# Kernel tuning notes

Measured on AMD Instinct MI355X. Metric: run time of the kernel, lower is better.

The kernel has to match this reference:

```python
import jax, jax.numpy as jnp
import numpy as np

N = 50000      # nodes
F_IN = 1024    # raw feature dim
D = 64         # student_dim = hidden_dim * compression_ratio
P = 3          # number of meta-paths
E = 1600000    # edges per meta-path adjacency (avg degree 32)


def setup_inputs() -> dict:
    key = jax.random.key(0)
    ks = jax.random.split(key, 10)
    feats = jax.random.normal(ks[0], (N, F_IN), jnp.float32)
    rows = jax.random.randint(ks[1], (P, E), 0, N, dtype=jnp.int32)
    cols = jax.random.randint(ks[2], (P, E), 0, N, dtype=jnp.int32)
    # normalized-adjacency-like positive edge weights
    vals = jax.random.uniform(ks[3], (P, E), jnp.float32) / 32.0
    # fc_list[0]: Linear(F_IN -> D), xavier_normal gain=1.414
    W0 = jax.random.normal(ks[4], (D, F_IN), jnp.float32) * 0.05
    b0 = jnp.zeros((D,), jnp.float32)
    # P GCN linear layers (D -> D, no bias) + GCN bias params
    Wg = jax.random.normal(ks[5], (P, D, D), jnp.float32) * 0.17
    bg = jnp.zeros((P, D), jnp.float32)
    # PReLU alpha (torch default init 0.25, one scalar per GCN)
    alpha = jnp.full((P,), 0.25, jnp.float32)
    # Attention: Linear(D -> D) and att vector [1, D]
    Wa = jax.random.normal(ks[6], (D, D), jnp.float32) * 0.17
    ba = jnp.zeros((D,), jnp.float32)
    att = jax.random.normal(ks[7], (1, D), jnp.float32) * 0.17
    return dict(feats=feats, rows=rows, cols=cols, vals=vals, W0=W0, b0=b0,
                Wg=Wg, bg=bg, alpha=alpha, Wa=Wa, ba=ba, att=att)


def reference(feats, rows, cols, vals, W0, b0, Wg, bg, alpha, Wa, ba, att):
    # h = elu(fc_list[0](feats))  (feat_drop = 0 -> identity)
    h = jax.nn.elu(feats @ W0.T + b0)                       # [N, D]
    embeds = []
    for i in range(P):
        s = h @ Wg[i].T                                     # [N, D]
        # sparse adj (COO) @ s : out[r] += v * s[c]
        msg = vals[i][:, None] * s[cols[i]]                 # [E, D]
        out = jax.ops.segment_sum(msg, rows[i], num_segments=N)
        out = out + bg[i]
        embeds.append(jnp.where(out > 0, out, alpha[i] * out))  # PReLU
    emb = jnp.stack(embeds)                                 # [P, N, D]
    # Attention over views: beta_i = att . mean_n tanh(fc(emb_i))
    sp = jnp.tanh(jnp.einsum('pnd,ed->pne', emb, Wa) + ba).mean(axis=1)  # [P, D]
    beta = jax.nn.softmax(sp @ att[0])                      # [P]
    z_mp = jnp.einsum('p,pnd->nd', beta, emb)               # [N, D]
    return z_mp
```

## Files before the change

### kernel.cpp

```cpp
#include <hip/hip_runtime.h>
#include <hip/hip_bf16.h>

#define N_NODES 50000
#define F_IN    1024
#define DD      64
#define PP      3
#define EE      1600000
#define NPC     98
#define CCAP    17664

typedef __attribute__((ext_vector_type(8))) short short8v;
typedef __attribute__((ext_vector_type(4))) float floatx4;
typedef __attribute__((ext_vector_type(2))) float floatx2;

__device__ inline float bfl(uint u) { return __uint_as_float(u << 16); }
__device__ inline float bfh(uint u) { return __uint_as_float(u & 0xffff0000u); }
__device__ inline floatx2 up2(uint u) {
    floatx2 r; r.x = bfl(u); r.y = bfh(u); return r;
}
__device__ inline uint cvtpk2(float a, float b) {
    __hip_bfloat162 h = __float22bfloat162_rn(make_float2(a, b));
    return *(uint*)&h;
}
__device__ inline ushort f2bf(float x) {
    __hip_bfloat16 h = __float2bfloat16(x);
    return *(ushort*)&h;
}

__global__ __launch_bounds__(256) void split_weights(const float* __restrict__ W0,
                                                     const float* __restrict__ Wg,
                                                     const float* __restrict__ Wa,
                                                     ushort* __restrict__ W0h,
                                                     ushort* __restrict__ Wgh,
                                                     ushort* __restrict__ Wah)
{
    int i = blockIdx.x * 256 + threadIdx.x;
    if (i < 64 * 1024) W0h[i] = f2bf(W0[i]);
    int j = i - 64 * 1024;
    if (j >= 0 && j < PP * 64 * 64) Wgh[j] = f2bf(Wg[j]);
    int k = i - 64 * 1024 - PP * 64 * 64;
    if (k >= 0 && k < 64 * 64) Wah[k] = f2bf(Wa[k]);
}

__global__ __launch_bounds__(256) void gemm1_fused(const float* __restrict__ feats,
                                                   const ushort* __restrict__ W0h,
                                                   const float* __restrict__ b0,
                                                   const ushort* __restrict__ Wgh,
                                                   ushort* __restrict__ s_all)
{
    __shared__ ushort Ah[64 * 64];
    __shared__ ushort Bh[64 * 64];
    const int t = threadIdx.x;
    const int w = t >> 6, lane = t & 63;
    const int row0 = blockIdx.x * 64;
    const int l15 = lane & 15, l4 = lane >> 4;

    floatx4 acc[4] = {};
    float4 pa[4];
    uint4  pb[2];

    #pragma unroll
    for (int rep = 0; rep < 4; ++rep) {
        int idx = rep * 256 + t;
        int r = idx >> 4, c4 = idx & 15;
        int gr = row0 + r; if (gr >= N_NODES) gr = N_NODES - 1;
        pa[rep] = *(const float4*)&feats[(size_t)gr * F_IN + c4 * 4];
    }
    #pragma unroll
    for (int rep = 0; rep < 2; ++rep) {
        int idx = rep * 256 + t;
        int c = idx >> 3, u8 = idx & 7;
        pb[rep] = *(const uint4*)&W0h[(size_t)c * F_IN + u8 * 8];
    }

    for (int kc = 0; kc < 16; ++kc) {
        #pragma unroll
        for (int rep = 0; rep < 4; ++rep) {
            int idx = rep * 256 + t;
            int r = idx >> 4, c4 = idx & 15;
            int unit = (c4 >> 1) ^ (r & 7);
            int base = r * 64 + unit * 8 + (c4 & 1) * 4;
            *(uint2*)&Ah[base] = make_uint2(cvtpk2(pa[rep].x, pa[rep].y),
                                            cvtpk2(pa[rep].z, pa[rep].w));
        }
        #pragma unroll
        for (int rep = 0; rep < 2; ++rep) {
            int idx = rep * 256 + t;
            int c = idx >> 3, u8 = idx & 7;
            int unit = u8 ^ (c & 7);
            *(uint4*)&Bh[c * 64 + unit * 8] = pb[rep];
        }
        __syncthreads();

        if (kc < 15) {
            #pragma unroll
            for (int rep = 0; rep < 4; ++rep) {
                int idx = rep * 256 + t;
                int r = idx >> 4, c4 = idx & 15;
                int gr = row0 + r; if (gr >= N_NODES) gr = N_NODES - 1;
                pa[rep] = *(const float4*)&feats[(size_t)gr * F_IN + (kc + 1) * 64 + c4 * 4];
            }
            #pragma unroll
            for (int rep = 0; rep < 2; ++rep) {
                int idx = rep * 256 + t;
                int c = idx >> 3, u8 = idx & 7;
                pb[rep] = *(const uint4*)&W0h[(size_t)c * F_IN + (kc + 1) * 64 + u8 * 8];
            }
        }

        #pragma unroll
        for (int ks = 0; ks < 2; ++ks) {
            int arow = w * 16 + l15;
            int au = (ks * 4 + l4) ^ (arow & 7);
            short8v ah = *(short8v*)&Ah[arow * 64 + au * 8];
            #pragma unroll
            for (int cf = 0; cf < 4; ++cf) {
                int bcol = cf * 16 + l15;
                int bu = (ks * 4 + l4) ^ (bcol & 7);
                short8v bh = *(short8v*)&Bh[bcol * 64 + bu * 8];
                acc[cf] = __builtin_amdgcn_mfma_f32_16x16x32_bf16(ah, bh, acc[cf], 0, 0, 0);
            }
        }
        __syncthreads();
    }

    #pragma unroll
    for (int cf = 0; cf < 4; ++cf) {
        int col = cf * 16 + l15;
        #pragma unroll
        for (int r = 0; r < 4; ++r) {
            int row = w * 16 + l4 * 4 + r;
            float x = acc[cf][r] + b0[col];
            x = x > 0.f ? x : (__expf(x) - 1.f);
            int u = (col >> 3) ^ (row & 7);
            Ah[row * 64 + u * 8 + (col & 7)] = f2bf(x);
        }
    }
    __syncthreads();

    for (int p = 0; p < PP; ++p) {
        #pragma unroll
        for (int rep = 0; rep < 2; ++rep) {
            int idx = rep * 256 + t;
            int r = idx >> 3, u8 = idx & 7;
            int unit = u8 ^ (r & 7);
            *(uint4*)&Bh[r * 64 + unit * 8] = *(const uint4*)&Wgh[(size_t)p * 4096 + idx * 8];
        }
        __syncthreads();

        floatx4 sacc[4] = {};
        #pragma unroll
        for (int ks = 0; ks < 2; ++ks) {
            int arow = w * 16 + l15;
            int au = (ks * 4 + l4) ^ (arow & 7);
            short8v ah = *(short8v*)&Ah[arow * 64 + au * 8];
            #pragma unroll
            for (int cf = 0; cf < 4; ++cf) {
                int bcol = cf * 16 + l15;
                int bu = (ks * 4 + l4) ^ (bcol & 7);
                short8v bh = *(short8v*)&Bh[bcol * 64 + bu * 8];
                sacc[cf] = __builtin_amdgcn_mfma_f32_16x16x32_bf16(ah, bh, sacc[cf], 0, 0, 0);
            }
        }
        ushort* sp = s_all + (size_t)p * N_NODES * 64;
        #pragma unroll
        for (int cf = 0; cf < 4; ++cf) {
            int col = cf * 16 + l15;
            #pragma unroll
            for (int r = 0; r < 4; ++r) {
                int gr = row0 + w * 16 + l4 * 4 + r;
                if (gr < N_NODES)
                    sp[(size_t)gr * 64 + col] = f2bf(sacc[cf][r]);
            }
        }
        __syncthreads();
    }
}

__global__ __launch_bounds__(256) void part1(const int*   __restrict__ rows,
                                             const int*   __restrict__ cols,
                                             const float* __restrict__ vals,
                                             int*   __restrict__ pcur3,
                                             uint2* __restrict__ coarsebuf)
{
    __shared__ uint2 stage[2560];
    __shared__ uint2 sorted[2560];
    __shared__ int cnt[128];
    __shared__ int sc[128];
    __shared__ int curb[128];
    __shared__ int gbase[128];
    const int t = threadIdx.x;
    const int path = blockIdx.y;
    const size_t ebase = (size_t)path * EE + (size_t)blockIdx.x * 2560;
    int* pcur = pcur3 + path * NPC;
    uint2* cb = coarsebuf + (size_t)path * NPC * CCAP;

    if (t < 128) { cnt[t] = 0; curb[t] = 0; }
    __syncthreads();

    #pragma unroll
    for (int it = 0; it < 10; ++it) {
        int e = it * 256 + t;
        int r = rows[ebase + e];
        int c = cols[ebase + e];
        float v = vals[ebase + e];
        int bin = r >> 9, rl = r & 511;
        stage[e] = make_uint2((uint)c | ((uint)rl << 16) | ((uint)bin << 25),
                              __float_as_uint(v));
        atomicAdd(&cnt[bin], 1);
    }
    __syncthreads();

    if (t < 128) sc[t] = cnt[t];
    __syncthreads();
    #pragma unroll
    for (int o = 1; o < 128; o <<= 1) {
        int v = (t < 128 && t >= o) ? sc[t - o] : 0;
        __syncthreads();
        if (t < 128 && t >= o) sc[t] += v;
        __syncthreads();
    }

    if (t < NPC) gbase[t] = atomicAdd(&pcur[t], cnt[t]);
    __syncthreads();

    #pragma unroll
    for (int it = 0; it < 10; ++it) {
        uint2 e = stage[it * 256 + t];
        int bin = e.x >> 25;
        int loc = (sc[bin] - cnt[bin]) + atomicAdd(&curb[bin], 1);
        sorted[loc] = e;
    }
    __syncthreads();

    #pragma unroll
    for (int it = 0; it < 10; ++it) {
        int i = it * 256 + t;
        uint2 e = sorted[i];
        int bin = e.x >> 25;
        int g = gbase[bin] + (i - (sc[bin] - cnt[bin]));
        if (g < CCAP) cb[(size_t)bin * CCAP + g] = e;
    }
}

__global__ __launch_bounds__(512) void sort2(const uint2* __restrict__ coarsebuf,
                                             const int*   __restrict__ pcur3,
                                             uint* __restrict__ sortpk,
                                             int* __restrict__ rowbeg3,
                                             int* __restrict__ rowend3)
{
    __shared__ int hist[512];
    __shared__ int cur[512];
    const int t = threadIdx.x;
    const int c = blockIdx.x, path = blockIdx.y;
    const int n = min(pcur3[path * NPC + c], CCAP);
    const size_t slabbase = ((size_t)path * NPC + c) * CCAP;
    const uint2* src = coarsebuf + slabbase;

    hist[t] = 0;
    __syncthreads();

    for (int i = t; i < n; i += 512)
        atomicAdd(&hist[(src[i].x >> 16) & 511], 1);
    __syncthreads();

    int c0 = hist[t];
    __syncthreads();
    #pragma unroll
    for (int o = 1; o < 512; o <<= 1) {
        int v = (t >= o) ? hist[t - o] : 0;
        __syncthreads();
        hist[t] += v;
        __syncthreads();
    }
    int excl = hist[t] - c0;
    cur[t] = excl;
    int gr = c * 512 + t;
    if (gr < N_NODES) {
        rowbeg3[path * N_NODES + gr] = (int)(slabbase + excl);
        rowend3[path * N_NODES + gr] = (int)(slabbase + excl + c0);
    }
    __syncthreads();

    for (int i = t; i < n; i += 512) {
        uint2 e = src[i];
        int rl = (e.x >> 16) & 511;
        int pos = atomicAdd(&cur[rl], 1);
        sortpk[slabbase + pos] = (e.x & 0xffffu) |
                                 ((uint)f2bf(__uint_as_float(e.y)) << 16);
    }
}

__global__ __launch_bounds__(256) void spmm_gather(const uint*   __restrict__ sortpk,
                                                   const int*    __restrict__ rowbeg3,
                                                   const int*    __restrict__ rowend3,
                                                   const ushort* __restrict__ s_all,
                                                   const float*  __restrict__ bg,
                                                   const float*  __restrict__ alpha,
                                                   ushort* __restrict__ emb)
{
    const int path = blockIdx.x / 12500;
    const int wid = (blockIdx.x % 12500) * 4 + (threadIdx.x >> 6);
    const int lane = threadIdx.x & 63;
    const int dq = lane & 7;
    const int slot = lane >> 3;
    const int e0 = rowbeg3[path * N_NODES + wid];
    const int e1 = rowend3[path * N_NODES + wid];
    const ushort* s_p = s_all + (size_t)path * N_NODES * 64;

    floatx2 acc[4] = {};
    if (e0 < e1) {
        const int last = e1 - 1;
        for (int e = e0; e < e1; e += 32) {
            int ea = e + slot, eb = ea + 8, ec = ea + 16, ed = ea + 24;
            uint pka = sortpk[min(ea, last)];
            uint pkb = sortpk[min(eb, last)];
            uint pkc = sortpk[min(ec, last)];
            uint pkd = sortpk[min(ed, last)];
            const uint4 ga = *(const uint4*)&s_p[(size_t)(pka & 0xffffu) * 64 + dq * 8];
            const uint4 gb = *(const uint4*)&s_p[(size_t)(pkb & 0xffffu) * 64 + dq * 8];
            const uint4 gc = *(const uint4*)&s_p[(size_t)(pkc & 0xffffu) * 64 + dq * 8];
            const uint4 gd = *(const uint4*)&s_p[(size_t)(pkd & 0xffffu) * 64 + dq * 8];
            float va = (ea <= last) ? bfh(pka) : 0.f;
            float vb = (eb <= last) ? bfh(pkb) : 0.f;
            float vc = (ec <= last) ? bfh(pkc) : 0.f;
            float vd = (ed <= last) ? bfh(pkd) : 0.f;
            floatx2 va2 = {va, va}, vb2 = {vb, vb}, vc2 = {vc, vc}, vd2 = {vd, vd};
            acc[0] += va2 * up2(ga.x); acc[1] += va2 * up2(ga.y);
            acc[2] += va2 * up2(ga.z); acc[3] += va2 * up2(ga.w);
            acc[0] += vb2 * up2(gb.x); acc[1] += vb2 * up2(gb.y);
            acc[2] += vb2 * up2(gb.z); acc[3] += vb2 * up2(gb.w);
            acc[0] += vc2 * up2(gc.x); acc[1] += vc2 * up2(gc.y);
            acc[2] += vc2 * up2(gc.z); acc[3] += vc2 * up2(gc.w);
            acc[0] += vd2 * up2(gd.x); acc[1] += vd2 * up2(gd.y);
            acc[2] += vd2 * up2(gd.z); acc[3] += vd2 * up2(gd.w);
        }
    }
    #pragma unroll
    for (int j = 0; j < 4; ++j) {
        acc[j].x += __shfl_xor(acc[j].x, 8);
        acc[j].y += __shfl_xor(acc[j].y, 8);
        acc[j].x += __shfl_xor(acc[j].x, 16);
        acc[j].y += __shfl_xor(acc[j].y, 16);
        acc[j].x += __shfl_xor(acc[j].x, 32);
        acc[j].y += __shfl_xor(acc[j].y, 32);
    }

    if (slot == 0) {
        const float al = alpha[path];
        const float* bgp = bg + path * 64;
        float x[8];
        #pragma unroll
        for (int j = 0; j < 4; ++j) {
            float v0 = acc[j].x + bgp[dq * 8 + 2 * j];
            float v1 = acc[j].y + bgp[dq * 8 + 2 * j + 1];
            x[2 * j]     = v0 > 0.f ? v0 : al * v0;
            x[2 * j + 1] = v1 > 0.f ? v1 : al * v1;
        }
        uint4 wv;
        wv.x = cvtpk2(x[0], x[1]);
        wv.y = cvtpk2(x[2], x[3]);
        wv.z = cvtpk2(x[4], x[5]);
        wv.w = cvtpk2(x[6], x[7]);
        *(uint4*)&emb[((size_t)path * N_NODES + wid) * 64 + dq * 8] = wv;
    }
}

__global__ __launch_bounds__(256) void postproc(const ushort* __restrict__ emb,
                                                const ushort* __restrict__ Wah,
                                                const float* __restrict__ ba,
                                                float* __restrict__ sp)
{
    __shared__ ushort Ah[64 * 64];
    __shared__ ushort Bh[64 * 64];
    __shared__ float red[16][64];
    const int t = threadIdx.x;
    const int w = t >> 6, lane = t & 63;
    const int l15 = lane & 15, l4 = lane >> 4;
    const int nb = (N_NODES + 63) >> 6;
    const int p  = blockIdx.x / nb;
    const int tb = blockIdx.x % nb;
    const int row0 = tb * 64;
    const ushort* embp = emb + (size_t)p * N_NODES * 64;

    #pragma unroll
    for (int rep = 0; rep < 2; ++rep) {
        int idx = rep * 256 + t;
        int r = idx >> 3, u8 = idx & 7;
        int gr = row0 + r; if (gr >= N_NODES) gr = N_NODES - 1;
        int unit = u8 ^ (r & 7);
        *(uint4*)&Ah[r * 64 + unit * 8] = *(const uint4*)&embp[(size_t)gr * 64 + u8 * 8];
        *(uint4*)&Bh[r * 64 + unit * 8] = *(const uint4*)&Wah[idx * 8];
    }
    __syncthreads();

    floatx4 acc[4] = {};
    #pragma unroll
    for (int ks = 0; ks < 2; ++ks) {
        int arow = w * 16 + l15;
        int au = (ks * 4 + l4) ^ (arow & 7);
        short8v ah = *(short8v*)&Ah[arow * 64 + au * 8];
        #pragma unroll
        for (int cf = 0; cf < 4; ++cf) {
            int bcol = cf * 16 + l15;
            int bu = (ks * 4 + l4) ^ (bcol & 7);
            short8v bh = *(short8v*)&Bh[bcol * 64 + bu * 8];
            acc[cf] = __builtin_amdgcn_mfma_f32_16x16x32_bf16(ah, bh, acc[cf], 0, 0, 0);
        }
    }

    #pragma unroll
    for (int cf = 0; cf < 4; ++cf) {
        int col = cf * 16 + l15;
        float s = 0.f;
        #pragma unroll
        for (int r = 0; r < 4; ++r) {
            int gr = row0 + w * 16 + l4 * 4 + r;
            if (gr < N_NODES) s += tanhf(acc[cf][r] + ba[col]);
        }
        red[w * 4 + l4][col] = s;
    }
    __syncthreads();
    if (t < 64) {
        float ssum = 0.f;
        #pragma unroll
        for (int g = 0; g < 16; ++g) ssum += red[g][t];
        unsafeAtomicAdd(&sp[p * 64 + t], ssum);
    }
}

__global__ void beta_kernel(const float* __restrict__ sp,
                            const float* __restrict__ att,
                            float* __restrict__ beta)
{
    int lane = threadIdx.x;
    float w[PP];
    #pragma unroll
    for (int p = 0; p < PP; ++p) {
        float x = sp[p * 64 + lane] * (1.0f / (float)N_NODES) * att[lane];
        #pragma unroll
        for (int off = 32; off; off >>= 1) x += __shfl_down(x, off);
        w[p] = __shfl(x, 0);
    }
    if (lane == 0) {
        float mx = fmaxf(w[0], fmaxf(w[1], w[2]));
        float e0 = __expf(w[0] - mx);
        float e1 = __expf(w[1] - mx);
        float e2 = __expf(w[2] - mx);
        float s = e0 + e1 + e2;
        beta[0] = e0 / s; beta[1] = e1 / s; beta[2] = e2 / s;
    }
}

__global__ __launch_bounds__(256) void combine(const ushort* __restrict__ emb,
                                               const float* __restrict__ beta,
                                               float* __restrict__ out)
{
    const float b0 = beta[0], b1 = beta[1], b2 = beta[2];
    const size_t tot = (size_t)N_NODES * 64;
    size_t i = ((size_t)blockIdx.x * 256 + threadIdx.x) * 8;
    if (i < tot) {
        uint4 e0 = *(const uint4*)&emb[i];
        uint4 e1 = *(const uint4*)&emb[tot + i];
        uint4 e2 = *(const uint4*)&emb[2 * tot + i];
        float o[8];
        o[0] = b0*bfl(e0.x) + b1*bfl(e1.x) + b2*bfl(e2.x);
        o[1] = b0*bfh(e0.x) + b1*bfh(e1.x) + b2*bfh(e2.x);
        o[2] = b0*bfl(e0.y) + b1*bfl(e1.y) + b2*bfl(e2.y);
        o[3] = b0*bfh(e0.y) + b1*bfh(e1.y) + b2*bfh(e2.y);
        o[4] = b0*bfl(e0.z) + b1*bfl(e1.z) + b2*bfl(e2.z);
        o[5] = b0*bfh(e0.z) + b1*bfh(e1.z) + b2*bfh(e2.z);
        o[6] = b0*bfl(e0.w) + b1*bfl(e1.w) + b2*bfl(e2.w);
        o[7] = b0*bfh(e0.w) + b1*bfh(e1.w) + b2*bfh(e2.w);
        *(float4*)&out[i]     = make_float4(o[0], o[1], o[2], o[3]);
        *(float4*)&out[i + 4] = make_float4(o[4], o[5], o[6], o[7]);
    }
}

extern "C" void kernel_launch(void* const* d_in, const int* in_sizes, int n_in,
                              void* d_out, int out_size, void* d_ws, size_t ws_size,
                              hipStream_t stream)
{
    const float* feats = (const float*)d_in[0];
    const int*   rows  = (const int*)  d_in[1];
    const int*   cols  = (const int*)  d_in[2];
    const float* vals  = (const float*)d_in[3];
    const float* W0    = (const float*)d_in[4];
    const float* b0    = (const float*)d_in[5];
    const float* Wg    = (const float*)d_in[6];
    const float* bg    = (const float*)d_in[7];
    const float* alpha = (const float*)d_in[8];
    const float* Wa    = (const float*)d_in[9];
    const float* ba    = (const float*)d_in[10];
    const float* att   = (const float*)d_in[11];
    float* out = (float*)d_out;

    const size_t ND = (size_t)N_NODES * 64;
    char* base = (char*)d_ws;
    ushort* emb    = (ushort*)base;              base += 3 * ND * 2;
    ushort* s_all  = (ushort*)base;              base += 3 * ND * 2;
    ushort* W0h    = (ushort*)base;              base += 64 * 1024 * 2;
    ushort* Wgh    = (ushort*)base;              base += PP * 64 * 64 * 2;
    ushort* Wah    = (ushort*)base;              base += 64 * 64 * 2;
    int*    pcur3  = (int*)base;                 base += PP * NPC * 4;
    float*  sp     = (float*)base;               base += 192 * 4;
    float*  beta   = (float*)base;               base += 64 * 4;
    int*    rowbeg3 = (int*)base;                base += PP * N_NODES * 4;
    int*    rowend3 = (int*)base;                base += PP * N_NODES * 4;
    base = (char*)(((size_t)base + 255) & ~(size_t)255);
    uint2*  coarsebuf = (uint2*)base;            base += (size_t)PP * NPC * CCAP * 8;
    uint*   sortpk    = (uint*)base;             base += (size_t)PP * NPC * CCAP * 4;

    hipMemsetAsync(pcur3, 0, (PP * NPC + 192) * sizeof(int), stream);

    split_weights<<<(64 * 1024 + PP * 64 * 64 + 64 * 64 + 255) / 256, 256, 0, stream>>>(
        W0, Wg, Wa, W0h, Wgh, Wah);

    gemm1_fused<<<782, 256, 0, stream>>>(feats, W0h, b0, Wgh, s_all);

    part1<<<dim3(EE / 2560, 3), 256, 0, stream>>>(rows, cols, vals, pcur3, coarsebuf);
    sort2<<<dim3(NPC, 3), 512, 0, stream>>>(coarsebuf, pcur3, sortpk, rowbeg3, rowend3);
    spmm_gather<<<3 * 12500, 256, 0, stream>>>(
        sortpk, rowbeg3, rowend3, s_all, bg, alpha, emb);

    postproc<<<3 * 782, 256, 0, stream>>>(emb, Wah, ba, sp);
    beta_kernel<<<1, 64, 0, stream>>>(sp, att, beta);
    combine<<<(int)((ND / 8 + 255) / 256), 256, 0, stream>>>(emb, beta, out);
}
```

Before: 316.8 us.

## Split first GEMM along K into two partial-sum blocks, combine in second kernel

The fused feats@W0 GEMM is split into two halves of the K=1024 dimension, launched as a 782x2 grid that writes fp32 partial tiles to a workspace buffer. A new combine kernel sums the partials, applies bias and ELU, and runs the three per-path 64x64 GEMMs. It also stages outputs through shared memory so they can be written as coalesced 16-byte stores. The aim is to double the block count for better CU occupancy on the bandwidth-bound feats read, at the cost of an extra kernel launch and about 25 MB of partial-sum traffic.

```diff
diff --git a/kernel.cpp b/kernel.cpp
--- a/kernel.cpp
+++ b/kernel.cpp
@@ -42,17 +42,16 @@
     if (k >= 0 && k < 64 * 64) Wah[k] = f2bf(Wa[k]);
 }
 
-__global__ __launch_bounds__(256) void gemm1_fused(const float* __restrict__ feats,
-                                                   const ushort* __restrict__ W0h,
-                                                   const float* __restrict__ b0,
-                                                   const ushort* __restrict__ Wgh,
-                                                   ushort* __restrict__ s_all)
+__global__ __launch_bounds__(256) void gemm1_partial(const float* __restrict__ feats,
+                                                     const ushort* __restrict__ W0h,
+                                                     float* __restrict__ hpart)
 {
     __shared__ ushort Ah[64 * 64];
     __shared__ ushort Bh[64 * 64];
     const int t = threadIdx.x;
     const int w = t >> 6, lane = t & 63;
     const int row0 = blockIdx.x * 64;
+    const int kh = blockIdx.y;
     const int l15 = lane & 15, l4 = lane >> 4;
 
     floatx4 acc[4] = {};
@@ -64,16 +63,16 @@
         int idx = rep * 256 + t;
         int r = idx >> 4, c4 = idx & 15;
         int gr = row0 + r; if (gr >= N_NODES) gr = N_NODES - 1;
-        pa[rep] = *(const float4*)&feats[(size_t)gr * F_IN + c4 * 4];
+        pa[rep] = *(const float4*)&feats[(size_t)gr * F_IN + (kh * 8) * 64 + c4 * 4];
     }
     #pragma unroll
     for (int rep = 0; rep < 2; ++rep) {
         int idx = rep * 256 + t;
         int c = idx >> 3, u8 = idx & 7;
-        pb[rep] = *(const uint4*)&W0h[(size_t)c * F_IN + u8 * 8];
-    }
-
-    for (int kc = 0; kc < 16; ++kc) {
+        pb[rep] = *(const uint4*)&W0h[(size_t)c * F_IN + (kh * 8) * 64 + u8 * 8];
+    }
+
+    for (int kc = 0; kc < 8; ++kc) {
         #pragma unroll
         for (int rep = 0; rep < 4; ++rep) {
             int idx = rep * 256 + t;
@@ -92,19 +91,20 @@
         }
         __syncthreads();
 
-        if (kc < 15) {
+        if (kc < 7) {
+            int g = kh * 8 + kc + 1;
             #pragma unroll
             for (int rep = 0; rep < 4; ++rep) {
                 int idx = rep * 256 + t;
                 int r = idx >> 4, c4 = idx & 15;
                 int gr = row0 + r; if (gr >= N_NODES) gr = N_NODES - 1;
-                pa[rep] = *(const float4*)&feats[(size_t)gr * F_IN + (kc + 1) * 64 + c4 * 4];
+                pa[rep] = *(const float4*)&feats[(size_t)gr * F_IN + g * 64 + c4 * 4];
             }
             #pragma unroll
             for (int rep = 0; rep < 2; ++rep) {
                 int idx = rep * 256 + t;
                 int c = idx >> 3, u8 = idx & 7;
-                pb[rep] = *(const uint4*)&W0h[(size_t)c * F_IN + (kc + 1) * 64 + u8 * 8];
+                pb[rep] = *(const uint4*)&W0h[(size_t)c * F_IN + g * 64 + u8 * 8];
             }
         }
 
@@ -124,13 +124,41 @@
         __syncthreads();
     }
 
+    float* hp = hpart + ((size_t)(kh * 782 + blockIdx.x)) * 4096;
+    #pragma unroll
+    for (int cf = 0; cf < 4; ++cf)
+        *(float4*)&hp[(cf * 256 + t) * 4] = make_float4(acc[cf][0], acc[cf][1],
+                                                        acc[cf][2], acc[cf][3]);
+}
+
+__global__ __launch_bounds__(256) void gemm2_combine(const float* __restrict__ hpart,
+                                                     const float* __restrict__ b0,
+                                                     const ushort* __restrict__ Wgh,
+                                                     ushort* __restrict__ s_all)
+{
+    __shared__ ushort Ah[64 * 64];
+    __shared__ ushort Bh[64 * 64];
+    __shared__ ushort Sout[64 * 64];
+    const int t = threadIdx.x;
+    const int w = t >> 6, lane = t & 63;
+    const int row0 = blockIdx.x * 64;
+    const int l15 = lane & 15, l4 = lane >> 4;
+
+    const float* hp0 = hpart + (size_t)blockIdx.x * 4096;
+    const float* hp1 = hpart + (size_t)(782 + blockIdx.x) * 4096;
+
     #pragma unroll
     for (int cf = 0; cf < 4; ++cf) {
+        float4 a = *(const float4*)&hp0[(cf * 256 + t) * 4];
+        float4 b = *(const float4*)&hp1[(cf * 256 + t) * 4];
         int col = cf * 16 + l15;
+        float bias = b0[col];
+        float xs[4] = {a.x + b.x + bias, a.y + b.y + bias,
+                       a.z + b.z + bias, a.w + b.w + bias};
         #pragma unroll
         for (int r = 0; r < 4; ++r) {
             int row = w * 16 + l4 * 4 + r;
-            float x = acc[cf][r] + b0[col];
+            float x = xs[r];
             x = x > 0.f ? x : (__expf(x) - 1.f);
             int u = (col >> 3) ^ (row & 7);
             Ah[row * 64 + u * 8 + (col & 7)] = f2bf(x);
@@ -162,15 +190,22 @@
                 sacc[cf] = __builtin_amdgcn_mfma_f32_16x16x32_bf16(ah, bh, sacc[cf], 0, 0, 0);
             }
         }
-        ushort* sp = s_all + (size_t)p * N_NODES * 64;
         #pragma unroll
         for (int cf = 0; cf < 4; ++cf) {
             int col = cf * 16 + l15;
             #pragma unroll
-            for (int r = 0; r < 4; ++r) {
-                int gr = row0 + w * 16 + l4 * 4 + r;
-                if (gr < N_NODES)
-                    sp[(size_t)gr * 64 + col] = f2bf(sacc[cf][r]);
+            for (int r = 0; r < 4; ++r)
+                Sout[(w * 16 + l4 * 4 + r) * 64 + col] = f2bf(sacc[cf][r]);
+        }
+        __syncthreads();
+        {
+            int lr = t >> 2;
+            int gr = row0 + lr;
+            if (gr < N_NODES) {
+                ushort* sp = s_all + (size_t)p * N_NODES * 64;
+                int co = (t & 3) * 16;
+                *(uint4*)&sp[(size_t)gr * 64 + co]     = *(uint4*)&Sout[lr * 64 + co];
+                *(uint4*)&sp[(size_t)gr * 64 + co + 8] = *(uint4*)&Sout[lr * 64 + co + 8];
             }
         }
         __syncthreads();
@@ -508,6 +543,7 @@
     int*    rowbeg3 = (int*)base;                base += PP * N_NODES * 4;
     int*    rowend3 = (int*)base;                base += PP * N_NODES * 4;
     base = (char*)(((size_t)base + 255) & ~(size_t)255);
+    float*  hpart  = (float*)base;               base += (size_t)2 * 782 * 4096 * 4;
     uint2*  coarsebuf = (uint2*)base;            base += (size_t)PP * NPC * CCAP * 8;
     uint*   sortpk    = (uint*)base;             base += (size_t)PP * NPC * CCAP * 4;
 
@@ -516,7 +552,8 @@
     split_weights<<<(64 * 1024 + PP * 64 * 64 + 64 * 64 + 255) / 256, 256, 0, stream>>>(
         W0, Wg, Wa, W0h, Wgh, Wah);
 
-    gemm1_fused<<<782, 256, 0, stream>>>(feats, W0h, b0, Wgh, s_all);
+    gemm1_partial<<<dim3(782, 2), 256, 0, stream>>>(feats, W0h, hpart);
+    gemm2_combine<<<782, 256, 0, stream>>>(hpart, b0, Wgh, s_all);
 
     part1<<<dim3(EE / 2560, 3), 256, 0, stream>>>(rows, cols, vals, pcur3, coarsebuf);
     sort2<<<dim3(NPC, 3), 512, 0, stream>>>(coarsebuf, pcur3, sortpk, rowbeg3, rowend3);
```

Result: no change. 319.4 us (+0.8%).
